# Kernel optimization log

Measured on AMD Instinct MI355X. Metric: run time of the kernel, lower is better.

Reference implementation:

```python
import jax, jax.numpy as jnp
import numpy as np

B, U, V = 2, 32, 2048
IN_DIM, STATE, CODE = 256, 512, 256
H, HD = 8, 64
INNER = H * HD  # 512
HID = STATE     # ffn capacity_factor = 1.0


def layernorm(x, g, b, eps=1e-5):
    mu = jnp.mean(x, axis=-1, keepdims=True)
    var = jnp.var(x, axis=-1, keepdims=True)
    return (x - mu) * jax.lax.rsqrt(var + eps) * g + b


def setup_inputs() -> dict:
    key = jax.random.key(0)
    ks = jax.random.split(key, 24)
    s = 0.02
    inp = {
        'receiver_states': jax.random.normal(ks[0], (B, U, STATE), jnp.float32),
        'receiver_signatures': jax.random.normal(ks[1], (B, U, 64), jnp.float32),
        'receiver_codes': jax.random.normal(ks[2], (B, U, CODE), jnp.float32),
        'sender_states': jax.random.normal(ks[3], (B, V, IN_DIM), jnp.float32),
        # layernorms
        'ln_s_g': jnp.ones((IN_DIM,), jnp.float32), 'ln_s_b': jnp.zeros((IN_DIM,), jnp.float32),
        'ln_r_g': jnp.ones((STATE,), jnp.float32), 'ln_r_b': jnp.zeros((STATE,), jnp.float32),
        # ModFC query: in=STATE out=INNER ctx=CODE
        'Wq': jax.random.normal(ks[4], (INNER, STATE), jnp.float32) * s,
        'bq': jnp.zeros((INNER,), jnp.float32),
        'Cq': jax.random.normal(ks[5], (STATE, CODE), jnp.float32) * s,
        # ModFC key/value: in=IN_DIM out=INNER ctx=CODE
        'Wk': jax.random.normal(ks[6], (INNER, IN_DIM), jnp.float32) * s,
        'bk': jnp.zeros((INNER,), jnp.float32),
        'Ck': jax.random.normal(ks[7], (IN_DIM, CODE), jnp.float32) * s,
        'Wv': jax.random.normal(ks[8], (INNER, IN_DIM), jnp.float32) * s,
        'bv': jnp.zeros((INNER,), jnp.float32),
        'Cv': jax.random.normal(ks[9], (IN_DIM, CODE), jnp.float32) * s,
        # exit ModFC: in=INNER out=STATE ctx=CODE
        'We': jax.random.normal(ks[10], (STATE, INNER), jnp.float32) * s,
        'be': jnp.zeros((STATE,), jnp.float32),
        'Ce': jax.random.normal(ks[11], (INNER, CODE), jnp.float32) * s,
        'ls_attn': jnp.ones((STATE,), jnp.float32) * 1.0,
        # FFN
        'ln_f_g': jnp.ones((STATE,), jnp.float32), 'ln_f_b': jnp.zeros((STATE,), jnp.float32),
        'W1': jax.random.normal(ks[12], (HID, STATE), jnp.float32) * s,
        'b1': jnp.zeros((HID,), jnp.float32),
        'C1': jax.random.normal(ks[13], (STATE, CODE), jnp.float32) * s,
        'W2': jax.random.normal(ks[14], (STATE, HID), jnp.float32) * s,
        'b2': jnp.zeros((STATE,), jnp.float32),
        'C2': jax.random.normal(ks[15], (HID, CODE), jnp.float32) * s,
        'ls_ffn': jnp.ones((STATE,), jnp.float32) * 1e-6,
    }
    return inp


def reference(receiver_states, receiver_signatures, receiver_codes, sender_states,
              ln_s_g, ln_s_b, ln_r_g, ln_r_b,
              Wq, bq, Cq, Wk, bk, Ck, Wv, bv, Cv, We, be, Ce, ls_attn,
              ln_f_g, ln_f_b, W1, b1, C1, W2, b2, C2, ls_ffn):
    codes = receiver_codes  # (b,u,code)
    # --- ReadInAttention ---
    r_ln = layernorm(receiver_states, ln_r_g, ln_r_b)           # (b,u,state)
    s_ln = layernorm(sender_states, ln_s_g, ln_s_b)             # (b,v,in)
    # ModFC: y = linear(x * (1 + code @ C))
    # queries: (b,u,inner)
    q = jnp.einsum('bus,is->bui', r_ln * (1.0 + jnp.einsum('buc,sc->bus', codes, Cq)), Wq) + bq
    # per-receiver modulated senders: scale (b,u,in) broadcast over v
    scale_k = 1.0 + jnp.einsum('buc,ic->bui', codes, Ck)        # (b,u,in)
    scale_v = 1.0 + jnp.einsum('buc,ic->bui', codes, Cv)        # (b,u,in)
    mod_k = s_ln[:, :, None, :] * scale_k[:, None, :, :]        # (b,v,u,in)
    mod_v = s_ln[:, :, None, :] * scale_v[:, None, :, :]        # (b,v,u,in)
    keys = jnp.einsum('bvui,oi->bvuo', mod_k, Wk) + bk          # (b,v,u,inner)
    values = jnp.einsum('bvui,oi->bvuo', mod_v, Wv) + bv        # (b,v,u,inner)
    keys = keys.reshape(B, V, U, H, HD).transpose(0, 3, 2, 1, 4)    # (b,h,u,v,c)
    values = values.reshape(B, V, U, H, HD).transpose(0, 3, 2, 1, 4)
    qh = q.reshape(B, U, H, HD).transpose(0, 2, 1, 3)           # (b,h,u,c)
    scores = jnp.einsum('bhuc,bhuvc->bhuv', qh, keys) / np.sqrt(HD)
    attn = jax.nn.softmax(scores, axis=-1)
    msg = jnp.einsum('bhuv,bhuvc->bhuc', attn, values)          # (b,h,u,c)
    msg = msg.transpose(0, 2, 1, 3).reshape(B, U, INNER)        # (b,u,inner)
    msg = jnp.einsum('bui,oi->buo', msg * (1.0 + jnp.einsum('buc,ic->bui', codes, Ce)), We) + be
    attn_out = msg * ls_attn  # include_residual=False in read-in attention
    # --- ModFFN (residual) ---
    x = attn_out
    r = layernorm(x, ln_f_g, ln_f_b)
    h1 = jnp.einsum('bus,os->buo', r * (1.0 + jnp.einsum('buc,sc->bus', codes, C1)), W1) + b1
    h1 = jax.nn.gelu(h1, approximate=False)
    h2 = jnp.einsum('buh,oh->buo', h1 * (1.0 + jnp.einsum('buc,hc->buh', codes, C2)), W2) + b2
    out = x + h2 * ls_ffn
    return out
```

## Files before the change

### kernel.cpp

```cpp
#include <hip/hip_runtime.h>
#include <math.h>

#define B_ 2
#define U_ 32
#define V_ 2048
#define IN_ 256
#define ST_ 512
#define H_ 8
#define BU_ 64
#define NR_ 512

#define WS_SLN   0u
#define WS_SLNT  1048576u
#define WS_SCALE 2097152u
#define WS_T     2260992u
#define WS_CB    2392064u
#define WS_SSUMP 2392576u
#define WS_CTXP  2396672u
#define WS_AO    3445248u
#define WS_H2    3478016u
#define WS_AOP   3510784u

__device__ __forceinline__ float wsum(float v){
  #pragma unroll
  for(int m=32;m>0;m>>=1) v += __shfl_xor(v, m, 64);
  return v;
}

#define FMA4(A, t, S) { A.x += (t)*(S).x; A.y += (t)*(S).y; A.z += (t)*(S).z; A.w += (t)*(S).w; }

__global__ __launch_bounds__(256) void k_pre(const float* __restrict__ snd,
    const float* __restrict__ g, const float* __restrict__ bb,
    const float* __restrict__ codes,
    const float* __restrict__ Cq, const float* __restrict__ Ck, const float* __restrict__ Cv,
    const float* __restrict__ Ce, const float* __restrict__ C1, const float* __restrict__ C2,
    float* __restrict__ ws){
  __shared__ float tile[32][261];
  __shared__ float cds[8][256];
  const int tid = threadIdx.x;
  if(blockIdx.x < 128){
    const int wave = tid>>6, lane = tid&63;
    const int rowbase = blockIdx.x * 32;
    const int b = rowbase >> 11, vloc = rowbase & 2047;
    float4 gg  = *(const float4*)(g  + lane*4);
    float4 bbv = *(const float4*)(bb + lane*4);
    for(int it=0; it<8; ++it){
      int rl = it*4 + wave;
      int r  = rowbase + rl;
      float4 x = *(const float4*)(snd + (size_t)r*IN_ + lane*4);
      float s = x.x+x.y+x.z+x.w;
      float q = x.x*x.x+x.y*x.y+x.z*x.z+x.w*x.w;
      s = wsum(s); q = wsum(q);
      float mu = s*(1.0f/256.0f);
      float rv = rsqrtf(q*(1.0f/256.0f) - mu*mu + 1e-5f);
      float4 y;
      y.x = (x.x-mu)*rv*gg.x + bbv.x;
      y.y = (x.y-mu)*rv*gg.y + bbv.y;
      y.z = (x.z-mu)*rv*gg.z + bbv.z;
      y.w = (x.w-mu)*rv*gg.w + bbv.w;
      *(float4*)(ws + WS_SLN + (size_t)r*IN_ + lane*4) = y;
      tile[rl][lane*4+0] = y.x;
      tile[rl][lane*4+1] = y.y;
      tile[rl][lane*4+2] = y.z;
      tile[rl][lane*4+3] = y.w;
    }
    __syncthreads();
    const int vh = tid & 31;
    const int ibase = (tid >> 5);
    for(int it=0; it<32; ++it){
      int i = it*8 + ibase;
      ws[WS_SLNT + ((size_t)b*IN_ + i)*V_ + vloc + vh] = tile[vh][i];
    }
  } else {
    const int idx = blockIdx.x - 128;
    const int cg = idx % 40, bg = idx / 40;
    #pragma unroll
    for(int j=0;j<8;++j){
      int fi = j*256 + tid;
      cds[fi>>8][fi&255] = codes[(size_t)(bg*8)*256 + fi];
    }
    __syncthreads();
    const int q = tid & 3;
    const int col = cg*64 + (tid >> 2);
    const float* Cp; int loc;
    if(col < 512){ Cp = Cq; loc = col; }
    else if(col < 768){ Cp = Ck; loc = col - 512; }
    else if(col < 1024){ Cp = Cv; loc = col - 768; }
    else if(col < 1536){ Cp = Ce; loc = col - 1024; }
    else if(col < 2048){ Cp = C1; loc = col - 1536; }
    else { Cp = C2; loc = col - 2048; }
    const float4* wrow = (const float4*)(Cp + (size_t)loc*256 + q*64);
    float acc[8] = {0,0,0,0,0,0,0,0};
    #pragma unroll 4
    for(int i=0;i<16;++i){
      float4 w = wrow[i];
      #pragma unroll
      for(int k=0;k<8;++k){
        const float4 c = *(const float4*)(&cds[k][q*64 + i*4]);
        acc[k] += w.x*c.x + w.y*c.y + w.z*c.z + w.w*c.w;
      }
    }
    #pragma unroll
    for(int k=0;k<8;++k){
      acc[k] += __shfl_xor(acc[k], 1, 64);
      acc[k] += __shfl_xor(acc[k], 2, 64);
    }
    ws[WS_SCALE + (size_t)(bg*8 + q)*2560 + col]     = 1.0f + acc[q];
    ws[WS_SCALE + (size_t)(bg*8 + q + 4)*2560 + col] = 1.0f + acc[q+4];
  }
}

__global__ __launch_bounds__(256) void k_qt(const float* __restrict__ rst,
    const float* __restrict__ lg, const float* __restrict__ lb,
    const float* __restrict__ Wq, const float* __restrict__ bq,
    const float* __restrict__ Wk, const float* __restrict__ bk,
    float* __restrict__ ws){
  const int bu = blockIdx.x >> 3, h = blockIdx.x & 7;
  const int b = bu >> 5, u = bu & 31;
  const int r = (b*8 + h)*32 + u;
  const int tid = threadIdx.x, wave = tid>>6, lane = tid&63;
  __shared__ float xm[512];
  __shared__ float qv[64];
  __shared__ float red[4][65];
  __shared__ float rsm[4], rqm[4];
  float2 x2 = *(const float2*)(rst + (size_t)bu*512 + tid*2);
  float s = x2.x + x2.y, q = x2.x*x2.x + x2.y*x2.y;
  s = wsum(s); q = wsum(q);
  if(lane==0){ rsm[wave] = s; rqm[wave] = q; }
  __syncthreads();
  float S = rsm[0]+rsm[1]+rsm[2]+rsm[3];
  float Q = rqm[0]+rqm[1]+rqm[2]+rqm[3];
  float mu = S*(1.0f/512.0f);
  float rv = rsqrtf(Q*(1.0f/512.0f) - mu*mu + 1e-5f);
  const float* scal = ws + WS_SCALE + (size_t)bu*2560;
  xm[tid*2]   = ((x2.x-mu)*rv*lg[tid*2]   + lb[tid*2])   * scal[tid*2];
  xm[tid*2+1] = ((x2.y-mu)*rv*lg[tid*2+1] + lb[tid*2+1]) * scal[tid*2+1];
  __syncthreads();
  {
    const int o = tid & 63, sp = tid >> 6;
    const float4* wq = (const float4*)(Wq + (size_t)(h*64 + o)*512 + sp*128);
    const float* xp = xm + sp*128;
    float acc = 0.f;
    #pragma unroll 8
    for(int c4=0;c4<32;++c4){
      float4 w = wq[c4];
      acc += w.x*xp[c4*4] + w.y*xp[c4*4+1] + w.z*xp[c4*4+2] + w.w*xp[c4*4+3];
    }
    red[sp][o] = acc;
  }
  __syncthreads();
  if(tid < 64)
    qv[tid] = red[0][tid]+red[1][tid]+red[2][tid]+red[3][tid] + bq[h*64+tid];
  __syncthreads();
  if(tid < 64){
    float p = qv[tid] * bk[h*64+tid];
    p = wsum(p);
    if(tid==0) ws[WS_CB + r] = p;
  }
  {
    float acc = 0.f;
    #pragma unroll 4
    for(int d=0; d<64; ++d)
      acc += qv[d] * Wk[(size_t)(h*64+d)*256 + tid];
    ws[WS_T + (size_t)r*256 + tid] = acc * scal[512 + tid];
  }
}

__global__ __launch_bounds__(512) void k_scctx(const float* __restrict__ Tm, float* __restrict__ ws){
  const int rg = blockIdx.x >> 3, vc = blockIdx.x & 7;
  const int r0 = rg * 8;
  const int b  = rg >> 5;
  const int v0 = vc * 256;
  const int tid = threadIdx.x, lane = tid & 63;
  const int w  = __builtin_amdgcn_readfirstlane(tid >> 6);
  const int wr = w & 1, wk = w >> 1;
  const int rw4 = wr * 4;
  const int i0 = lane * 4;
  const int srow = tid >> 6;
  const int sf   = (tid & 63) * 4;

  __shared__ float P[8][256];
  __shared__ float stg[2][32][256];

  float4 a0={0,0,0,0},a1={0,0,0,0},a2={0,0,0,0},a3={0,0,0,0};
  const float* Trow = Tm + (size_t)(r0 + rw4)*256;

  const float* p1base = ws + WS_SLNT + (size_t)b*IN_*V_ + v0;
  float4 g0,g1,g2,g3;
  g0 = *(const float4*)(p1base + (size_t)(srow    )*V_ + sf);
  g1 = *(const float4*)(p1base + (size_t)(srow+ 8)*V_ + sf);
  g2 = *(const float4*)(p1base + (size_t)(srow+16)*V_ + sf);
  g3 = *(const float4*)(p1base + (size_t)(srow+24)*V_ + sf);
  for(int s=0; s<8; ++s){
    float (*sb)[256] = stg[s&1];
    *(float4*)&sb[srow   ][sf] = g0;
    *(float4*)&sb[srow+ 8][sf] = g1;
    *(float4*)&sb[srow+16][sf] = g2;
    *(float4*)&sb[srow+24][sf] = g3;
    if(s < 7){
      const float* nb = p1base + (size_t)(s+1)*32*V_;
      g0 = *(const float4*)(nb + (size_t)(srow    )*V_ + sf);
      g1 = *(const float4*)(nb + (size_t)(srow+ 8)*V_ + sf);
      g2 = *(const float4*)(nb + (size_t)(srow+16)*V_ + sf);
      g3 = *(const float4*)(nb + (size_t)(srow+24)*V_ + sf);
    }
    const int kgA = s*32 + wk*8;
    float4 tA[4], tB[4];
    #pragma unroll
    for(int j=0;j<4;++j) tA[j] = *(const float4*)(Trow + (size_t)j*256 + kgA);
    #pragma unroll
    for(int j=0;j<4;++j) tB[j] = *(const float4*)(Trow + (size_t)j*256 + kgA + 4);
    __syncthreads();
    {
      const int kl = wk*8;
      float4 s0 = *(const float4*)&sb[kl+0][i0];
      float4 s1 = *(const float4*)&sb[kl+1][i0];
      float4 s2 = *(const float4*)&sb[kl+2][i0];
      float4 s3 = *(const float4*)&sb[kl+3][i0];
      FMA4(a0,tA[0].x,s0) FMA4(a0,tA[0].y,s1) FMA4(a0,tA[0].z,s2) FMA4(a0,tA[0].w,s3)
      FMA4(a1,tA[1].x,s0) FMA4(a1,tA[1].y,s1) FMA4(a1,tA[1].z,s2) FMA4(a1,tA[1].w,s3)
      FMA4(a2,tA[2].x,s0) FMA4(a2,tA[2].y,s1) FMA4(a2,tA[2].z,s2) FMA4(a2,tA[2].w,s3)
      FMA4(a3,tA[3].x,s0) FMA4(a3,tA[3].y,s1) FMA4(a3,tA[3].z,s2) FMA4(a3,tA[3].w,s3)
    }
    {
      const int kl = wk*8 + 4;
      float4 s0 = *(const float4*)&sb[kl+0][i0];
      float4 s1 = *(const float4*)&sb[kl+1][i0];
      float4 s2 = *(const float4*)&sb[kl+2][i0];
      float4 s3 = *(const float4*)&sb[kl+3][i0];
      FMA4(a0,tB[0].x,s0) FMA4(a0,tB[0].y,s1) FMA4(a0,tB[0].z,s2) FMA4(a0,tB[0].w,s3)
      FMA4(a1,tB[1].x,s0) FMA4(a1,tB[1].y,s1) FMA4(a1,tB[1].z,s2) FMA4(a1,tB[1].w,s3)
      FMA4(a2,tB[2].x,s0) FMA4(a2,tB[2].y,s1) FMA4(a2,tB[2].z,s2) FMA4(a2,tB[2].w,s3)
      FMA4(a3,tB[3].x,s0) FMA4(a3,tB[3].y,s1) FMA4(a3,tB[3].z,s2) FMA4(a3,tB[3].w,s3)
    }
  }
  __syncthreads();
  if(wk == 0){
    *(float4*)&P[rw4+0][i0]=a0; *(float4*)&P[rw4+1][i0]=a1;
    *(float4*)&P[rw4+2][i0]=a2; *(float4*)&P[rw4+3][i0]=a3;
  } else if(wk == 1){
    *(float4*)&stg[0][rw4+0][i0]=a0; *(float4*)&stg[0][rw4+1][i0]=a1;
    *(float4*)&stg[0][rw4+2][i0]=a2; *(float4*)&stg[0][rw4+3][i0]=a3;
  } else if(wk == 2){
    *(float4*)&stg[0][8+rw4+0][i0]=a0; *(float4*)&stg[0][8+rw4+1][i0]=a1;
    *(float4*)&stg[0][8+rw4+2][i0]=a2; *(float4*)&stg[0][8+rw4+3][i0]=a3;
  }
  __syncthreads();
  if(wk == 3){
    float4 av[4] = {a0,a1,a2,a3};
    #pragma unroll
    for(int j=0;j<4;++j){
      const int r = r0 + rw4 + j;
      const float cb = ws[WS_CB + r];
      float4 q0 = *(const float4*)&P[rw4+j][i0];
      float4 q1 = *(const float4*)&stg[0][rw4+j][i0];
      float4 q2 = *(const float4*)&stg[0][8+rw4+j][i0];
      float4 e;
      e.x = __expf((av[j].x+q0.x+q1.x+q2.x+cb)*0.125f);
      e.y = __expf((av[j].y+q0.y+q1.y+q2.y+cb)*0.125f);
      e.z = __expf((av[j].z+q0.z+q1.z+q2.z+cb)*0.125f);
      e.w = __expf((av[j].w+q0.w+q1.w+q2.w+cb)*0.125f);
      *(float4*)&P[rw4+j][i0] = e;
      float ss = wsum(e.x+e.y+e.z+e.w);
      if(lane==0) ws[WS_SSUMP + (size_t)r*8 + vc] = ss;
    }
  }
  __syncthreads();

  a0=make_float4(0,0,0,0); a1=a0; a2=a0; a3=a0;
  const float* p2base = ws + WS_SLN + ((size_t)b*V_ + v0)*IN_;
  g0 = *(const float4*)(p2base + (size_t)(srow    )*IN_ + sf);
  g1 = *(const float4*)(p2base + (size_t)(srow+ 8)*IN_ + sf);
  g2 = *(const float4*)(p2base + (size_t)(srow+16)*IN_ + sf);
  g3 = *(const float4*)(p2base + (size_t)(srow+24)*IN_ + sf);
  for(int sv=0; sv<8; ++sv){
    float (*sb)[256] = stg[sv&1];
    *(float4*)&sb[srow   ][sf] = g0;
    *(float4*)&sb[srow+ 8][sf] = g1;
    *(float4*)&sb[srow+16][sf] = g2;
    *(float4*)&sb[srow+24][sf] = g3;
    if(sv < 7){
      const float* nb = p2base + (size_t)(sv+1)*32*IN_;
      g0 = *(const float4*)(nb + (size_t)(srow    )*IN_ + sf);
      g1 = *(const float4*)(nb + (size_t)(srow+ 8)*IN_ + sf);
      g2 = *(const float4*)(nb + (size_t)(srow+16)*IN_ + sf);
      g3 = *(const float4*)(nb + (size_t)(srow+24)*IN_ + sf);
    }
    __syncthreads();
    #pragma unroll
    for(int half=0; half<2; ++half){
      const int vl = wk*8 + half*4, vg = sv*32 + vl;
      float4 p0_ = *(const float4*)&P[rw4+0][vg];
      float4 p1_ = *(const float4*)&P[rw4+1][vg];
      float4 p2_ = *(const float4*)&P[rw4+2][vg];
      float4 p3_ = *(const float4*)&P[rw4+3][vg];
      float4 s0 = *(const float4*)&sb[vl+0][i0];
      float4 s1 = *(const float4*)&sb[vl+1][i0];
      float4 s2 = *(const float4*)&sb[vl+2][i0];
      float4 s3 = *(const float4*)&sb[vl+3][i0];
      FMA4(a0,p0_.x,s0) FMA4(a0,p0_.y,s1) FMA4(a0,p0_.z,s2) FMA4(a0,p0_.w,s3)
      FMA4(a1,p1_.x,s0) FMA4(a1,p1_.y,s1) FMA4(a1,p1_.z,s2) FMA4(a1,p1_.w,s3)
      FMA4(a2,p2_.x,s0) FMA4(a2,p2_.y,s1) FMA4(a2,p2_.z,s2) FMA4(a2,p2_.w,s3)
      FMA4(a3,p3_.x,s0) FMA4(a3,p3_.y,s1) FMA4(a3,p3_.z,s2) FMA4(a3,p3_.w,s3)
    }
  }
  __syncthreads();
  if(wk == 0){
    *(float4*)&P[rw4+0][i0]=a0; *(float4*)&P[rw4+1][i0]=a1;
    *(float4*)&P[rw4+2][i0]=a2; *(float4*)&P[rw4+3][i0]=a3;
  } else if(wk == 1){
    *(float4*)&stg[0][rw4+0][i0]=a0; *(float4*)&stg[0][rw4+1][i0]=a1;
    *(float4*)&stg[0][rw4+2][i0]=a2; *(float4*)&stg[0][rw4+3][i0]=a3;
  } else if(wk == 2){
    *(float4*)&stg[0][8+rw4+0][i0]=a0; *(float4*)&stg[0][8+rw4+1][i0]=a1;
    *(float4*)&stg[0][8+rw4+2][i0]=a2; *(float4*)&stg[0][8+rw4+3][i0]=a3;
  }
  __syncthreads();
  if(wk == 3){
    float4 av[4] = {a0,a1,a2,a3};
    #pragma unroll
    for(int j=0;j<4;++j){
      const int r = r0 + rw4 + j;
      float4 q0 = *(const float4*)&P[rw4+j][i0];
      float4 q1 = *(const float4*)&stg[0][rw4+j][i0];
      float4 q2 = *(const float4*)&stg[0][8+rw4+j][i0];
      float4 d;
      d.x = av[j].x+q0.x+q1.x+q2.x;
      d.y = av[j].y+q0.y+q1.y+q2.y;
      d.z = av[j].z+q0.z+q1.z+q2.z;
      d.w = av[j].w+q0.w+q1.w+q2.w;
      *(float4*)(ws + WS_CTXP + ((size_t)vc*NR_ + r)*IN_ + i0) = d;
    }
  }
}

__global__ __launch_bounds__(512) void k_mexit(const float* __restrict__ Wv, const float* __restrict__ bv,
    const float* __restrict__ We, float* __restrict__ ws){
  const int bu = blockIdx.x >> 2, st = blockIdx.x & 3;
  const int b = bu >> 5, u = bu & 31;
  const int tid = threadIdx.x;
  __shared__ float xs[2][256];
  __shared__ float m2s[128];
  __shared__ float ps[4][128];
  __shared__ float invS[2];
  if(tid < 2){
    const int r = (b*8 + st*2 + tid)*32 + u;
    float v = 0.f;
    #pragma unroll
    for(int k=0;k<8;++k) v += ws[WS_SSUMP + (size_t)r*8 + k];
    invS[tid] = 1.0f / v;
  }
  {
    const int hh = tid >> 8, i = tid & 255;
    const int r = (b*8 + st*2 + hh)*32 + u;
    float s = 0.f;
    #pragma unroll
    for(int vcx=0; vcx<8; ++vcx)
      s += ws[WS_CTXP + ((size_t)vcx*NR_ + r)*IN_ + i];
    xs[hh][i] = s * ws[WS_SCALE + (size_t)bu*2560 + 768 + i];
  }
  __syncthreads();
  {
    const int lo = tid & 127, sp = tid >> 7;
    const int o = st*128 + lo;
    const float4* wv = (const float4*)(Wv + (size_t)o*256 + sp*64);
    const float* xp = &xs[lo>>6][sp*64];
    float acc = 0.f;
    #pragma unroll
    for(int c4=0;c4<16;++c4){
      float4 w = wv[c4];
      acc += w.x*xp[c4*4]+w.y*xp[c4*4+1]+w.z*xp[c4*4+2]+w.w*xp[c4*4+3];
    }
    ps[sp][lo] = acc;
  }
  __syncthreads();
  if(tid < 128){
    const int o = st*128 + tid;
    m2s[tid] = ((ps[0][tid]+ps[1][tid]+ps[2][tid]+ps[3][tid]) * invS[tid>>6] + bv[o])
               * ws[WS_SCALE + (size_t)bu*2560 + 1024 + o];
  }
  __syncthreads();
  {
    const float4* we = (const float4*)(We + (size_t)tid*512 + st*128);
    float acc = 0.f;
    #pragma unroll 8
    for(int c4=0;c4<32;++c4){
      float4 w = we[c4];
      acc += w.x*m2s[c4*4]+w.y*m2s[c4*4+1]+w.z*m2s[c4*4+2]+w.w*m2s[c4*4+3];
    }
    ws[WS_AOP + ((size_t)st*BU_ + bu)*512 + tid] = acc;
  }
}

__global__ __launch_bounds__(256) void k_ffn1(const float* __restrict__ be, const float* __restrict__ lsa,
    const float* __restrict__ lg, const float* __restrict__ lb,
    const float* __restrict__ W1, const float* __restrict__ b1, float* __restrict__ ws){
  const int bu = blockIdx.x >> 2, ot = blockIdx.x & 3;
  const int tid = threadIdx.x, wave = tid>>6, lane = tid&63;
  __shared__ float xr[512];
  __shared__ float rsm[4], rqm[4];
  __shared__ float ps[2][128];
  const int s2 = tid*2;
  float2 x2;
  {
    const float* aop = ws + WS_AOP;
    float2 a0 = *(const float2*)(aop + ((size_t)0*BU_+bu)*512+s2);
    float2 a1 = *(const float2*)(aop + ((size_t)1*BU_+bu)*512+s2);
    float2 a2 = *(const float2*)(aop + ((size_t)2*BU_+bu)*512+s2);
    float2 a3 = *(const float2*)(aop + ((size_t)3*BU_+bu)*512+s2);
    x2.x = (a0.x+a1.x+a2.x+a3.x + be[s2])   * lsa[s2];
    x2.y = (a0.y+a1.y+a2.y+a3.y + be[s2+1]) * lsa[s2+1];
    *(float2*)(ws + WS_AO + (size_t)bu*512 + s2) = x2;
  }
  float s = x2.x+x2.y, q = x2.x*x2.x+x2.y*x2.y;
  s = wsum(s); q = wsum(q);
  if(lane==0){ rsm[wave]=s; rqm[wave]=q; }
  __syncthreads();
  float S=rsm[0]+rsm[1]+rsm[2]+rsm[3], Q=rqm[0]+rqm[1]+rqm[2]+rqm[3];
  float mu = S*(1.0f/512.0f);
  float rv = rsqrtf(Q*(1.0f/512.0f) - mu*mu + 1e-5f);
  const float* scal = ws + WS_SCALE + (size_t)bu*2560;
  xr[s2]   = ((x2.x-mu)*rv*lg[s2]   + lb[s2])   * scal[1536 + s2];
  xr[s2+1] = ((x2.y-mu)*rv*lg[s2+1] + lb[s2+1]) * scal[1536 + s2+1];
  __syncthreads();
  const int o = ot*128 + (tid & 127), sp = tid >> 7;
  const float4* w1 = (const float4*)(W1 + (size_t)o*512 + sp*256);
  const float* xp = xr + sp*256;
  float acc = 0.f;
  #pragma unroll 8
  for(int c4=0;c4<64;++c4){
    float4 w = w1[c4];
    acc += w.x*xp[c4*4]+w.y*xp[c4*4+1]+w.z*xp[c4*4+2]+w.w*xp[c4*4+3];
  }
  ps[sp][tid&127] = acc;
  __syncthreads();
  if(sp==0){
    float hh = ps[0][tid] + ps[1][tid] + b1[o];
    float ge = 0.5f*hh*(1.0f + erff(hh*0.70710678118654752f));
    ws[WS_H2 + (size_t)bu*512 + o] = ge * scal[2048 + o];
  }
}

__global__ __launch_bounds__(256) void k_ffn2(const float* __restrict__ W2, const float* __restrict__ b2,
    const float* __restrict__ lsf, const float* __restrict__ ws, float* __restrict__ out){
  const int bu = blockIdx.x >> 2, st = blockIdx.x & 3;
  const int tid = threadIdx.x;
  const int s = st*128 + (tid & 127), sp = tid >> 7;
  __shared__ float ps[2][128];
  const float4* w2 = (const float4*)(W2 + (size_t)s*512 + sp*256);
  const float* hp = ws + WS_H2 + (size_t)bu*512 + sp*256;
  float acc = 0.f;
  #pragma unroll 8
  for(int c4=0;c4<64;++c4){
    float4 w = w2[c4];
    acc += w.x*hp[c4*4]+w.y*hp[c4*4+1]+w.z*hp[c4*4+2]+w.w*hp[c4*4+3];
  }
  ps[sp][tid&127] = acc;
  __syncthreads();
  if(sp==0)
    out[(size_t)bu*512 + s] = ws[WS_AO + (size_t)bu*512 + s]
                            + (ps[0][tid]+ps[1][tid] + b2[s]) * lsf[s];
}

extern "C" void kernel_launch(void* const* d_in, const int* in_sizes, int n_in,
                              void* d_out, int out_size, void* d_ws, size_t ws_size,
                              hipStream_t stream) {
  (void)in_sizes; (void)n_in; (void)out_size; (void)ws_size;
  const float* rst   = (const float*)d_in[0];
  const float* codes = (const float*)d_in[2];
  const float* snd   = (const float*)d_in[3];
  const float* ln_s_g = (const float*)d_in[4];
  const float* ln_s_b = (const float*)d_in[5];
  const float* ln_r_g = (const float*)d_in[6];
  const float* ln_r_b = (const float*)d_in[7];
  const float* Wq = (const float*)d_in[8];
  const float* bq = (const float*)d_in[9];
  const float* Cq = (const float*)d_in[10];
  const float* Wk = (const float*)d_in[11];
  const float* bk = (const float*)d_in[12];
  const float* Ck = (const float*)d_in[13];
  const float* Wv = (const float*)d_in[14];
  const float* bv = (const float*)d_in[15];
  const float* Cv = (const float*)d_in[16];
  const float* We = (const float*)d_in[17];
  const float* be = (const float*)d_in[18];
  const float* Ce = (const float*)d_in[19];
  const float* lsa = (const float*)d_in[20];
  const float* ln_f_g = (const float*)d_in[21];
  const float* ln_f_b = (const float*)d_in[22];
  const float* W1 = (const float*)d_in[23];
  const float* b1 = (const float*)d_in[24];
  const float* C1 = (const float*)d_in[25];
  const float* W2 = (const float*)d_in[26];
  const float* b2 = (const float*)d_in[27];
  const float* C2 = (const float*)d_in[28];
  const float* lsf = (const float*)d_in[29];
  float* ws  = (float*)d_ws;
  float* out = (float*)d_out;

  k_pre   <<<448, 256, 0, stream>>>(snd, ln_s_g, ln_s_b, codes, Cq, Ck, Cv, Ce, C1, C2, ws);
  k_qt    <<<512, 256, 0, stream>>>(rst, ln_r_g, ln_r_b, Wq, bq, Wk, bk, ws);
  k_scctx <<<512, 512, 0, stream>>>((const float*)(ws + WS_T), ws);
  k_mexit <<<256, 512, 0, stream>>>(Wv, bv, We, ws);
  k_ffn1  <<<256, 256, 0, stream>>>(be, lsa, ln_f_g, ln_f_b, W1, b1, ws);
  k_ffn2  <<<256, 256, 0, stream>>>(W2, b2, lsf, ws, out);
}
```

Before: 93.03 us.

## Split k_scctx reduction across eight waves with each wave covering all rows

Changes the k_scctx warp decomposition so each of the eight waves owns all eight rows and a four-wide slice of the reduction dimension, instead of four rows and an eight-wide slice. Each shared-memory staging value loaded is now reused across eight rows, which cuts LDS reads per FMA. In exchange each thread holds twice as many accumulators, and the cross-wave reduction grows from four to eight partials, using both staging buffers as scratch. The final sum is done by a single wave, which serializes more of the work in the epilogue.

```diff
diff --git a/kernel.cpp b/kernel.cpp
--- a/kernel.cpp
+++ b/kernel.cpp
@@ -172,9 +172,7 @@
   const int b  = rg >> 5;
   const int v0 = vc * 256;
   const int tid = threadIdx.x, lane = tid & 63;
-  const int w  = __builtin_amdgcn_readfirstlane(tid >> 6);
-  const int wr = w & 1, wk = w >> 1;
-  const int rw4 = wr * 4;
+  const int wk = __builtin_amdgcn_readfirstlane(tid >> 6);
   const int i0 = lane * 4;
   const int srow = tid >> 6;
   const int sf   = (tid & 63) * 4;
@@ -182,8 +180,10 @@
   __shared__ float P[8][256];
   __shared__ float stg[2][32][256];
 
-  float4 a0={0,0,0,0},a1={0,0,0,0},a2={0,0,0,0},a3={0,0,0,0};
-  const float* Trow = Tm + (size_t)(r0 + rw4)*256;
+  float4 a[8];
+  #pragma unroll
+  for(int j=0;j<8;++j) a[j] = make_float4(0,0,0,0);
+  const float* Trow = Tm + (size_t)r0*256;
 
   const float* p1base = ws + WS_SLNT + (size_t)b*IN_*V_ + v0;
   float4 g0,g1,g2,g3;
@@ -204,70 +204,68 @@
       g2 = *(const float4*)(nb + (size_t)(srow+16)*V_ + sf);
       g3 = *(const float4*)(nb + (size_t)(srow+24)*V_ + sf);
     }
-    const int kgA = s*32 + wk*8;
-    float4 tA[4], tB[4];
-    #pragma unroll
-    for(int j=0;j<4;++j) tA[j] = *(const float4*)(Trow + (size_t)j*256 + kgA);
-    #pragma unroll
-    for(int j=0;j<4;++j) tB[j] = *(const float4*)(Trow + (size_t)j*256 + kgA + 4);
+    const int kg = s*32 + wk*4;
+    float4 t0 = *(const float4*)(Trow + 0*256 + kg);
+    float4 t1 = *(const float4*)(Trow + 1*256 + kg);
+    float4 t2 = *(const float4*)(Trow + 2*256 + kg);
+    float4 t3 = *(const float4*)(Trow + 3*256 + kg);
     __syncthreads();
-    {
-      const int kl = wk*8;
-      float4 s0 = *(const float4*)&sb[kl+0][i0];
-      float4 s1 = *(const float4*)&sb[kl+1][i0];
-      float4 s2 = *(const float4*)&sb[kl+2][i0];
-      float4 s3 = *(const float4*)&sb[kl+3][i0];
-      FMA4(a0,tA[0].x,s0) FMA4(a0,tA[0].y,s1) FMA4(a0,tA[0].z,s2) FMA4(a0,tA[0].w,s3)
-      FMA4(a1,tA[1].x,s0) FMA4(a1,tA[1].y,s1) FMA4(a1,tA[1].z,s2) FMA4(a1,tA[1].w,s3)
-      FMA4(a2,tA[2].x,s0) FMA4(a2,tA[2].y,s1) FMA4(a2,tA[2].z,s2) FMA4(a2,tA[2].w,s3)
-      FMA4(a3,tA[3].x,s0) FMA4(a3,tA[3].y,s1) FMA4(a3,tA[3].z,s2) FMA4(a3,tA[3].w,s3)
-    }
-    {
-      const int kl = wk*8 + 4;
-      float4 s0 = *(const float4*)&sb[kl+0][i0];
-      float4 s1 = *(const float4*)&sb[kl+1][i0];
-      float4 s2 = *(const float4*)&sb[kl+2][i0];
-      float4 s3 = *(const float4*)&sb[kl+3][i0];
-      FMA4(a0,tB[0].x,s0) FMA4(a0,tB[0].y,s1) FMA4(a0,tB[0].z,s2) FMA4(a0,tB[0].w,s3)
-      FMA4(a1,tB[1].x,s0) FMA4(a1,tB[1].y,s1) FMA4(a1,tB[1].z,s2) FMA4(a1,tB[1].w,s3)
-      FMA4(a2,tB[2].x,s0) FMA4(a2,tB[2].y,s1) FMA4(a2,tB[2].z,s2) FMA4(a2,tB[2].w,s3)
-      FMA4(a3,tB[3].x,s0) FMA4(a3,tB[3].y,s1) FMA4(a3,tB[3].z,s2) FMA4(a3,tB[3].w,s3)
-    }
+    const int kl = wk*4;
+    float4 s0 = *(const float4*)&sb[kl+0][i0];
+    float4 s1 = *(const float4*)&sb[kl+1][i0];
+    float4 s2 = *(const float4*)&sb[kl+2][i0];
+    float4 s3 = *(const float4*)&sb[kl+3][i0];
+    FMA4(a[0],t0.x,s0) FMA4(a[0],t0.y,s1) FMA4(a[0],t0.z,s2) FMA4(a[0],t0.w,s3)
+    FMA4(a[1],t1.x,s0) FMA4(a[1],t1.y,s1) FMA4(a[1],t1.z,s2) FMA4(a[1],t1.w,s3)
+    FMA4(a[2],t2.x,s0) FMA4(a[2],t2.y,s1) FMA4(a[2],t2.z,s2) FMA4(a[2],t2.w,s3)
+    FMA4(a[3],t3.x,s0) FMA4(a[3],t3.y,s1) FMA4(a[3],t3.z,s2) FMA4(a[3],t3.w,s3)
+    t0 = *(const float4*)(Trow + 4*256 + kg);
+    t1 = *(const float4*)(Trow + 5*256 + kg);
+    t2 = *(const float4*)(Trow + 6*256 + kg);
+    t3 = *(const float4*)(Trow + 7*256 + kg);
+    FMA4(a[4],t0.x,s0) FMA4(a[4],t0.y,s1) FMA4(a[4],t0.z,s2) FMA4(a[4],t0.w,s3)
+    FMA4(a[5],t1.x,s0) FMA4(a[5],t1.y,s1) FMA4(a[5],t1.z,s2) FMA4(a[5],t1.w,s3)
+    FMA4(a[6],t2.x,s0) FMA4(a[6],t2.y,s1) FMA4(a[6],t2.z,s2) FMA4(a[6],t2.w,s3)
+    FMA4(a[7],t3.x,s0) FMA4(a[7],t3.y,s1) FMA4(a[7],t3.z,s2) FMA4(a[7],t3.w,s3)
   }
   __syncthreads();
   if(wk == 0){
-    *(float4*)&P[rw4+0][i0]=a0; *(float4*)&P[rw4+1][i0]=a1;
-    *(float4*)&P[rw4+2][i0]=a2; *(float4*)&P[rw4+3][i0]=a3;
-  } else if(wk == 1){
-    *(float4*)&stg[0][rw4+0][i0]=a0; *(float4*)&stg[0][rw4+1][i0]=a1;
-    *(float4*)&stg[0][rw4+2][i0]=a2; *(float4*)&stg[0][rw4+3][i0]=a3;
-  } else if(wk == 2){
-    *(float4*)&stg[0][8+rw4+0][i0]=a0; *(float4*)&stg[0][8+rw4+1][i0]=a1;
-    *(float4*)&stg[0][8+rw4+2][i0]=a2; *(float4*)&stg[0][8+rw4+3][i0]=a3;
-  }
-  __syncthreads();
-  if(wk == 3){
-    float4 av[4] = {a0,a1,a2,a3};
-    #pragma unroll
-    for(int j=0;j<4;++j){
-      const int r = r0 + rw4 + j;
+    #pragma unroll
+    for(int j=0;j<8;++j) *(float4*)&P[j][i0] = a[j];
+  } else if(wk <= 4){
+    #pragma unroll
+    for(int j=0;j<8;++j) *(float4*)&stg[0][(wk-1)*8 + j][i0] = a[j];
+  } else if(wk <= 6){
+    #pragma unroll
+    for(int j=0;j<8;++j) *(float4*)&stg[1][(wk-5)*8 + j][i0] = a[j];
+  }
+  __syncthreads();
+  if(wk == 7){
+    #pragma unroll
+    for(int j=0;j<8;++j){
+      const int r = r0 + j;
       const float cb = ws[WS_CB + r];
-      float4 q0 = *(const float4*)&P[rw4+j][i0];
-      float4 q1 = *(const float4*)&stg[0][rw4+j][i0];
-      float4 q2 = *(const float4*)&stg[0][8+rw4+j][i0];
+      float4 q0 = *(const float4*)&P[j][i0];
+      float4 q1 = *(const float4*)&stg[0][ 0+j][i0];
+      float4 q2 = *(const float4*)&stg[0][ 8+j][i0];
+      float4 q3 = *(const float4*)&stg[0][16+j][i0];
+      float4 q4 = *(const float4*)&stg[0][24+j][i0];
+      float4 q5 = *(const float4*)&stg[1][ 0+j][i0];
+      float4 q6 = *(const float4*)&stg[1][ 8+j][i0];
       float4 e;
-      e.x = __expf((av[j].x+q0.x+q1.x+q2.x+cb)*0.125f);
-      e.y = __expf((av[j].y+q0.y+q1.y+q2.y+cb)*0.125f);
-      e.z = __expf((av[j].z+q0.z+q1.z+q2.z+cb)*0.125f);
-      e.w = __expf((av[j].w+q0.w+q1.w+q2.w+cb)*0.125f);
-      *(float4*)&P[rw4+j][i0] = e;
+      e.x = __expf((a[j].x+q0.x+q1.x+q2.x+q3.x+q4.x+q5.x+q6.x+cb)*0.125f);
+      e.y = __expf((a[j].y+q0.y+q1.y+q2.y+q3.y+q4.y+q5.y+q6.y+cb)*0.125f);
+      e.z = __expf((a[j].z+q0.z+q1.z+q2.z+q3.z+q4.z+q5.z+q6.z+cb)*0.125f);
+      e.w = __expf((a[j].w+q0.w+q1.w+q2.w+q3.w+q4.w+q5.w+q6.w+cb)*0.125f);
+      *(float4*)&P[j][i0] = e;
       float ss = wsum(e.x+e.y+e.z+e.w);
       if(lane==0) ws[WS_SSUMP + (size_t)r*8 + vc] = ss;
     }
   }
   __syncthreads();
 
-  a0=make_float4(0,0,0,0); a1=a0; a2=a0; a3=a0;
+  #pragma unroll
+  for(int j=0;j<8;++j) a[j] = make_float4(0,0,0,0);
   const float* p2base = ws + WS_SLN + ((size_t)b*V_ + v0)*IN_;
   g0 = *(const float4*)(p2base + (size_t)(srow    )*IN_ + sf);
   g1 = *(const float4*)(p2base + (size_t)(srow+ 8)*IN_ + sf);
@@ -287,48 +285,56 @@
       g3 = *(const float4*)(nb + (size_t)(srow+24)*IN_ + sf);
     }
     __syncthreads();
-    #pragma unroll
-    for(int half=0; half<2; ++half){
-      const int vl = wk*8 + half*4, vg = sv*32 + vl;
-      float4 p0_ = *(const float4*)&P[rw4+0][vg];
-      float4 p1_ = *(const float4*)&P[rw4+1][vg];
-      float4 p2_ = *(const float4*)&P[rw4+2][vg];
-      float4 p3_ = *(const float4*)&P[rw4+3][vg];
-      float4 s0 = *(const float4*)&sb[vl+0][i0];
-      float4 s1 = *(const float4*)&sb[vl+1][i0];
-      float4 s2 = *(const float4*)&sb[vl+2][i0];
-      float4 s3 = *(const float4*)&sb[vl+3][i0];
-      FMA4(a0,p0_.x,s0) FMA4(a0,p0_.y,s1) FMA4(a0,p0_.z,s2) FMA4(a0,p0_.w,s3)
-      FMA4(a1,p1_.x,s0) FMA4(a1,p1_.y,s1) FMA4(a1,p1_.z,s2) FMA4(a1,p1_.w,s3)
-      FMA4(a2,p2_.x,s0) FMA4(a2,p2_.y,s1) FMA4(a2,p2_.z,s2) FMA4(a2,p2_.w,s3)
-      FMA4(a3,p3_.x,s0) FMA4(a3,p3_.y,s1) FMA4(a3,p3_.z,s2) FMA4(a3,p3_.w,s3)
-    }
+    const int vl = wk*4, vg = sv*32 + vl;
+    float4 s0 = *(const float4*)&sb[vl+0][i0];
+    float4 s1 = *(const float4*)&sb[vl+1][i0];
+    float4 s2 = *(const float4*)&sb[vl+2][i0];
+    float4 s3 = *(const float4*)&sb[vl+3][i0];
+    float4 p0 = *(const float4*)&P[0][vg];
+    float4 p1 = *(const float4*)&P[1][vg];
+    float4 p2 = *(const float4*)&P[2][vg];
+    float4 p3 = *(const float4*)&P[3][vg];
+    FMA4(a[0],p0.x,s0) FMA4(a[0],p0.y,s1) FMA4(a[0],p0.z,s2) FMA4(a[0],p0.w,s3)
+    FMA4(a[1],p1.x,s0) FMA4(a[1],p1.y,s1) FMA4(a[1],p1.z,s2) FMA4(a[1],p1.w,s3)
+    FMA4(a[2],p2.x,s0) FMA4(a[2],p2.y,s1) FMA4(a[2],p2.z,s2) FMA4(a[2],p2.w,s3)
+    FMA4(a[3],p3.x,s0) FMA4(a[3],p3.y,s1) FMA4(a[3],p3.z,s2) FMA4(a[3],p3.w,s3)
+    p0 = *(const float4*)&P[4][vg];
+    p1 = *(const float4*)&P[5][vg];
+    p2 = *(const float4*)&P[6][vg];
+    p3 = *(const float4*)&P[7][vg];
+    FMA4(a[4],p0.x,s0) FMA4(a[4],p0.y,s1) FMA4(a[4],p0.z,s2) FMA4(a[4],p0.w,s3)
+    FMA4(a[5],p1.x,s0) FMA4(a[5],p1.y,s1) FMA4(a[5],p1.z,s2) FMA4(a[5],p1.w,s3)
+    FMA4(a[6],p2.x,s0) FMA4(a[6],p2.y,s1) FMA4(a[6],p2.z,s2) FMA4(a[6],p2.w,s3)
+    FMA4(a[7],p3.x,s0) FMA4(a[7],p3.y,s1) FMA4(a[7],p3.z,s2) FMA4(a[7],p3.w,s3)
   }
   __syncthreads();
   if(wk == 0){
-    *(float4*)&P[rw4+0][i0]=a0; *(float4*)&P[rw4+1][i0]=a1;
-    *(float4*)&P[rw4+2][i0]=a2; *(float4*)&P[rw4+3][i0]=a3;
-  } else if(wk == 1){
-    *(float4*)&stg[0][rw4+0][i0]=a0; *(float4*)&stg[0][rw4+1][i0]=a1;
-    *(float4*)&stg[0][rw4+2][i0]=a2; *(float4*)&stg[0][rw4+3][i0]=a3;
-  } else if(wk == 2){
-    *(float4*)&stg[0][8+rw4+0][i0]=a0; *(float4*)&stg[0][8+rw4+1][i0]=a1;
-    *(float4*)&stg[0][8+rw4+2][i0]=a2; *(float4*)&stg[0][8+rw4+3][i0]=a3;
-  }
-  __syncthreads();
-  if(wk == 3){
-    float4 av[4] = {a0,a1,a2,a3};
-    #pragma unroll
-    for(int j=0;j<4;++j){
-      const int r = r0 + rw4 + j;
-      float4 q0 = *(const float4*)&P[rw4+j][i0];
-      float4 q1 = *(const float4*)&stg[0][rw4+j][i0];
-      float4 q2 = *(const float4*)&stg[0][8+rw4+j][i0];
+    #pragma unroll
+    for(int j=0;j<8;++j) *(float4*)&P[j][i0] = a[j];
+  } else if(wk <= 4){
+    #pragma unroll
+    for(int j=0;j<8;++j) *(float4*)&stg[0][(wk-1)*8 + j][i0] = a[j];
+  } else if(wk <= 6){
+    #pragma unroll
+    for(int j=0;j<8;++j) *(float4*)&stg[1][(wk-5)*8 + j][i0] = a[j];
+  }
+  __syncthreads();
+  if(wk == 7){
+    #pragma unroll
+    for(int j=0;j<8;++j){
+      const int r = r0 + j;
+      float4 q0 = *(const float4*)&P[j][i0];
+      float4 q1 = *(const float4*)&stg[0][ 0+j][i0];
+      float4 q2 = *(const float4*)&stg[0][ 8+j][i0];
+      float4 q3 = *(const float4*)&stg[0][16+j][i0];
+      float4 q4 = *(const float4*)&stg[0][24+j][i0];
+      float4 q5 = *(const float4*)&stg[1][ 0+j][i0];
+      float4 q6 = *(const float4*)&stg[1][ 8+j][i0];
       float4 d;
-      d.x = av[j].x+q0.x+q1.x+q2.x;
-      d.y = av[j].y+q0.y+q1.y+q2.y;
-      d.z = av[j].z+q0.z+q1.z+q2.z;
-      d.w = av[j].w+q0.w+q1.w+q2.w;
+      d.x = a[j].x+q0.x+q1.x+q2.x+q3.x+q4.x+q5.x+q6.x;
+      d.y = a[j].y+q0.y+q1.y+q2.y+q3.y+q4.y+q5.y+q6.y;
+      d.z = a[j].z+q0.z+q1.z+q2.z+q3.z+q4.z+q5.z+q6.z;
+      d.w = a[j].w+q0.w+q1.w+q2.w+q3.w+q4.w+q5.w+q6.w;
       *(float4*)(ws + WS_CTXP + ((size_t)vc*NR_ + r)*IN_ + i0) = d;
     }
   }
```

Result: slower. 95.63 us (+2.8%).
